# Optimization experiments

Measured on AMD Instinct MI355X. Metric: run time of the kernel, lower is better.

The kernel has to match this reference:

```python
import jax, jax.numpy as jnp
import numpy as np

B, N, NODE_DIM, EMB, T = 16, 256, 5, 128, 4


def _linear_params(key, din, dout):
    kw, kb = jax.random.split(key)
    s = 1.0 / np.sqrt(din)
    w = jax.random.uniform(kw, (din, dout), minval=-s, maxval=s, dtype=jnp.float32)
    b = jax.random.uniform(kb, (dout,), minval=-s, maxval=s, dtype=jnp.float32)
    return w, b


def setup_inputs() -> dict:
    key = jax.random.key(0)
    ks = jax.random.split(key, 10)
    inp = {
        "xv": jax.random.normal(ks[0], (B, N, NODE_DIM), dtype=jnp.float32),
        "Ws": jax.random.uniform(ks[1], (B, N, N), dtype=jnp.float32),
    }
    inp["t1_w"], inp["t1_b"] = _linear_params(ks[2], NODE_DIM, EMB)
    inp["t2_w"], inp["t2_b"] = _linear_params(ks[3], EMB, EMB)
    inp["t3_w"], inp["t3_b"] = _linear_params(ks[4], EMB, EMB)
    inp["t4_w"], inp["t4_b"] = _linear_params(ks[5], 1, EMB)
    inp["t5_w"], inp["t5_b"] = _linear_params(ks[6], 2 * EMB, 1)
    inp["t6_w"], inp["t6_b"] = _linear_params(ks[7], EMB, EMB)
    inp["t7_w"], inp["t7_b"] = _linear_params(ks[8], EMB, EMB)
    inp["layer_w"], inp["layer_b"] = _linear_params(ks[9], EMB, EMB)
    return inp


def reference(xv, Ws, t1_w, t1_b, t2_w, t2_b, t3_w, t3_b, t4_w, t4_b,
              t5_w, t5_b, t6_w, t6_b, t7_w, t7_b, layer_w, layer_b):
    batch, num_nodes = xv.shape[0], xv.shape[1]
    emb = t1_w.shape[1]
    conn = (Ws > 0).astype(xv.dtype)  # [B,N,N]
    # s1 = layer(relu(theta1(xv)))
    s1 = jnp.maximum(xv @ t1_w + t1_b, 0.0) @ layer_w + layer_b  # [B,N,E]
    # s3 = theta3(sum_i relu(theta4(Ws[:,i,j,None])))
    s3_1 = jnp.maximum(Ws[..., None] * t4_w[0] + t4_b, 0.0)  # [B,N,N,E]
    s3 = s3_1.sum(axis=1) @ t3_w + t3_b  # [B,N,E]
    mu = jnp.zeros((batch, num_nodes, emb), dtype=xv.dtype)
    for _ in range(T):
        s2 = jnp.matmul(conn, mu) @ t2_w + t2_b  # [B,N,E]
        mu = jnp.maximum(s1 + s2 + s3, 0.0)
    # global state: theta6 applied to pooled mu, broadcast to all nodes
    global_state = mu.sum(axis=1, keepdims=True) @ t6_w + t6_b  # [B,1,E]
    global_state = jnp.broadcast_to(global_state, mu.shape)  # [B,N,E]
    local_action = mu @ t7_w + t7_b  # [B,N,E]
    out = jnp.maximum(jnp.concatenate([global_state, local_action], axis=2), 0.0)
    return (out @ t5_w + t5_b).squeeze(2)  # [B,N]
```

## Files before the change

### kernel.cpp

```cpp
#include <hip/hip_runtime.h>

#define BATCH 16
#define NN    256
#define E     128
#define NR    (BATCH*NN)
#define ZCAP  8
#define KP    132
#define MAGIC 0x7F3A2B1C

typedef float f4 __attribute__((ext_vector_type(4)));

__global__ __launch_bounds__(1024) void k_all(
    const float* __restrict__ xv,  const float* __restrict__ Ws,
    const float* __restrict__ t1w, const float* __restrict__ t1b,
    const float* __restrict__ t2w, const float* __restrict__ t2b,
    const float* __restrict__ t3w, const float* __restrict__ t3b,
    const float* __restrict__ t4w, const float* __restrict__ t4b,
    const float* __restrict__ t5w, const float* __restrict__ t5b,
    const float* __restrict__ t6w, const float* __restrict__ t6b,
    const float* __restrict__ t7w, const float* __restrict__ t7b,
    const float* __restrict__ lw,  const float* __restrict__ lb,
    float* __restrict__ s13g, float* __restrict__ zmu4g,
    float* __restrict__ s2b3g, float* __restrict__ gsumG,
    int* __restrict__ zcnt, int* __restrict__ doneA, int* __restrict__ flagA,
    float* __restrict__ out)
{
    (void)zmu4g; (void)s2b3g; (void)gsumG; (void)flagA;

    const int blk = blockIdx.x;
    const int b   = blk >> 4;
    const int bt  = blk & 15;
    const int j0  = bt * 16;
    const int r0  = b*NN + j0;
    const int t   = threadIdx.x;
    const int e   = t & 127;
    const int q   = t >> 7;
    const size_t bb = (size_t)b*NN*E;

    __shared__ __align__(16) float s3l[16][KP];
    __shared__ __align__(16) float hsl[16][KP];
    __shared__ __align__(16) float s13l[16][E];
    __shared__ __align__(16) float sQA[8][E];
    __shared__ __align__(16) float sQB[8][E];
    __shared__ __align__(16) float dbuf[E], s2bL[E];
    __shared__ float zmuP[ZCAP][E], zmuN[ZCAP][E];
    __shared__ int   zmap[NN];
    __shared__ int   zlist[ZCAP];
    __shared__ int   nzs;
    __shared__ int   lcnt[16];
    __shared__ float sredO[16][2];
    __shared__ float sg2[2];

    const float* wb = Ws + (size_t)b*NN*NN;
    if (t < 16) lcnt[t] = 0;

    {
        const int jl = t & 15, s = t >> 4;
        const int e4 = (s & 31) * 4, ipart = s >> 5;
        float a0=t4w[e4],a1=t4w[e4+1],a2=t4w[e4+2],a3=t4w[e4+3];
        float c0=t4b[e4],c1=t4b[e4+1],c2=t4b[e4+2],c3=t4b[e4+3];
        float x0=0,x1=0,x2=0,x3=0;
        const float* p = wb + (size_t)(ipart*128)*NN + j0 + jl;
        #pragma unroll 8
        for (int i = 0; i < 128; ++i) {
            float w = p[(size_t)i*NN];
            x0 += fmaxf(w*a0 + c0, 0.f);
            x1 += fmaxf(w*a1 + c1, 0.f);
            x2 += fmaxf(w*a2 + c2, 0.f);
            x3 += fmaxf(w*a3 + c3, 0.f);
        }
        __syncthreads();
        if (ipart == 0) {
            f4 v; v.x=x0; v.y=x1; v.z=x2; v.w=x3;
            *(f4*)&s3l[jl][e4] = v;
        }
        __syncthreads();
        if (ipart == 1) {
            f4 v = *(const f4*)&s3l[jl][e4];
            v.x+=x0; v.y+=x1; v.z+=x2; v.w+=x3;
            *(f4*)&s3l[jl][e4] = v;
        }
    }
    {
        float b1 = t1b[e];
        float w0=t1w[e],w1=t1w[E+e],w2=t1w[2*E+e],w3=t1w[3*E+e],w4=t1w[4*E+e];
        #pragma unroll
        for (int rr = 0; rr < 2; ++rr) {
            const float* x = xv + (size_t)(r0 + q*2 + rr)*5;
            hsl[q*2+rr][e] =
                fmaxf(b1 + x[0]*w0+x[1]*w1+x[2]*w2+x[3]*w3+x[4]*w4, 0.f);
        }
    }
    {
        const int rw = t >> 6, l = t & 63;
        f4 w = *(const f4*)(wb + (size_t)(j0 + rw)*NN + l*4);
        int c = (w.x<=0.f) + (w.y<=0.f) + (w.z<=0.f) + (w.w<=0.f);
        if (c) atomicAdd(&lcnt[rw], c);
    }
    __syncthreads();
    {
        const int jp = q*2;
        float acc0 = 0.f, acc1 = 0.f;
        #pragma unroll 2
        for (int k0 = 0; k0 < E; k0 += 4) {
            f4 h0 = *(const f4*)&hsl[jp][k0];
            f4 h1 = *(const f4*)&hsl[jp+1][k0];
            f4 s0 = *(const f4*)&s3l[jp][k0];
            f4 s1 = *(const f4*)&s3l[jp+1][k0];
            #pragma unroll
            for (int m = 0; m < 4; ++m) {
                float wl = lw[(k0+m)*E + e], w3 = t3w[(k0+m)*E + e];
                acc0 += h0[m]*wl + s0[m]*w3;
                acc1 += h1[m]*wl + s1[m]*w3;
            }
        }
        float bb2 = lb[e] + t3b[e];
        float v0 = acc0 + bb2, v1 = acc1 + bb2;
        s13l[jp][e] = v0;  s13l[jp+1][e] = v1;
        __hip_atomic_store(&s13g[(size_t)(r0+jp)*E + e],   v0,
                           __ATOMIC_RELAXED, __HIP_MEMORY_SCOPE_AGENT);
        __hip_atomic_store(&s13g[(size_t)(r0+jp+1)*E + e], v1,
                           __ATOMIC_RELAXED, __HIP_MEMORY_SCOPE_AGENT);
    }
    if (t < 16)
        __hip_atomic_store(&zcnt[r0 + t], lcnt[t],
                           __ATOMIC_RELAXED, __HIP_MEMORY_SCOPE_AGENT);
    __syncthreads();
    if (t == 0)
        __hip_atomic_store(&doneA[b*16 + bt], MAGIC,
                           __ATOMIC_RELEASE, __HIP_MEMORY_SCOPE_AGENT);

    if (t == 0) {
        int ok = 0, spins = 0;
        while (ok < 16 && spins < (1 << 18)) {
            ok = 0;
            #pragma unroll
            for (int i = 0; i < 16; ++i)
                ok += (__hip_atomic_load(&doneA[b*16+i], __ATOMIC_RELAXED,
                                         __HIP_MEMORY_SCOPE_AGENT) == MAGIC);
            if (ok < 16) __builtin_amdgcn_s_sleep(2);
            ++spins;
        }
        (void)__hip_atomic_load(&doneA[b*16], __ATOMIC_ACQUIRE,
                                __HIP_MEMORY_SCOPE_AGENT);
        nzs = 0;
    }
    if (t < NN) zmap[t] = -1;
    __syncthreads();
    if (t < NN) {
        if (__hip_atomic_load(&zcnt[b*NN + t], __ATOMIC_RELAXED,
                              __HIP_MEMORY_SCOPE_AGENT) > 0) {
            int s = atomicAdd(&nzs, 1);
            if (s < ZCAP) { zlist[s] = t; zmap[t] = s; }
        }
    }
    __syncthreads();
    const int nz = nzs < ZCAP ? nzs : ZCAP;

    float reg[32];
    #pragma unroll
    for (int j = 0; j < 32; ++j)
        reg[j] = __hip_atomic_load(&s13g[bb + (size_t)(q*32+j)*E + e],
                                   __ATOMIC_RELAXED, __HIP_MEMORY_SCOPE_AGENT);

    float s2b_r  = t2b[e];
    float s2bP_r = s2b_r;

    for (int it = 0; it < 4; ++it) {
        if (nz > 0) {
            if (q == 0) s2bL[e] = s2b_r;
            __syncthreads();
            for (int z = 0; z < nz; ++z) {
                int j = zlist[z];
                float cp = 0.f;
                const float* wr = wb + (size_t)j*NN;
                if (it > 0) {
                    #pragma unroll
                    for (int u = 0; u < 32; ++u) {
                        int i = q*32 + u;
                        if (wr[i] <= 0.f) {
                            int zi = zmap[i];
                            cp += (zi >= 0) ? zmuP[zi][e]
                                            : fmaxf(reg[u] + s2bP_r, 0.f);
                        }
                    }
                }
                sQA[q][e] = cp;
                __syncthreads();
                if (q == 0) {
                    float s = 0.f;
                    #pragma unroll
                    for (int qq = 0; qq < 8; ++qq) s += sQA[qq][e];
                    dbuf[e] = s;
                }
                __syncthreads();
                float cb = 0.f;
                #pragma unroll 2
                for (int k = 0; k < E; k += 4) {
                    f4 d = *(const f4*)&dbuf[k];
                    cb += d.x*t2w[(k+0)*E+e] + d.y*t2w[(k+1)*E+e]
                        + d.z*t2w[(k+2)*E+e] + d.w*t2w[(k+3)*E+e];
                }
                if (q == 0) {
                    float sj = __hip_atomic_load(&s13g[bb+(size_t)j*E+e],
                                  __ATOMIC_RELAXED, __HIP_MEMORY_SCOPE_AGENT);
                    zmuN[z][e] = fmaxf(sj + s2b_r - cb, 0.f);
                }
                __syncthreads();
            }
        }

        float csp = 0.f;
        #pragma unroll
        for (int u = 0; u < 32; ++u) csp += fmaxf(reg[u] + s2b_r, 0.f);
        sQA[q][e] = csp;
        __syncthreads();

        const float* W = (it < 3) ? t2w : t6w;
        float pa = 0.f;
        #pragma unroll
        for (int g4 = 0; g4 < 4; ++g4) {
            const int k0 = q*16 + g4*4;
            f4 c = *(const f4*)&sQA[0][k0];
            #pragma unroll
            for (int qq = 1; qq < 8; ++qq) {
                f4 d = *(const f4*)&sQA[qq][k0];
                c.x += d.x; c.y += d.y; c.z += d.z; c.w += d.w;
            }
            if (nz > 0) {
                for (int z = 0; z < nz; ++z) {
                    int j = zlist[z];
                    #pragma unroll
                    for (int m = 0; m < 4; ++m) {
                        float sj = __hip_atomic_load(
                            &s13g[bb+(size_t)j*E + k0 + m],
                            __ATOMIC_RELAXED, __HIP_MEMORY_SCOPE_AGENT);
                        c[m] += zmuN[z][k0+m] - fmaxf(sj + s2bL[k0+m], 0.f);
                    }
                }
            }
            pa += c.x*W[(k0+0)*E+e] + c.y*W[(k0+1)*E+e]
                + c.z*W[(k0+2)*E+e] + c.w*W[(k0+3)*E+e];
        }
        sQB[q][e] = pa;
        s2bP_r = s2b_r;
        if (nz > 0 && q == 0)
            for (int z = 0; z < nz; ++z) zmuP[z][e] = zmuN[z][e];
        __syncthreads();

        if (it < 3) {
            float s = t2b[e];
            #pragma unroll
            for (int qq = 0; qq < 8; ++qq) s += sQB[qq][e];
            s2b_r = s;
        }
    }

    if (q == 0) {
        float g = t6b[e];
        #pragma unroll
        for (int qq = 0; qq < 8; ++qq) g += sQB[qq][e];
        float v = fmaxf(g, 0.f) * t5w[e];
        #pragma unroll
        for (int off = 32; off; off >>= 1) v += __shfl_down(v, off, 64);
        if ((t & 63) == 0) sg2[t >> 6] = v;
    }
    {
        #pragma unroll
        for (int rr = 0; rr < 2; ++rr) {
            int row = q*2 + rr;
            int zi  = zmap[j0 + row];
            float v = (zi >= 0) ? zmuP[zi][e]
                                : fmaxf(s13l[row][e] + s2b_r, 0.f);
            hsl[row][e] = v;
        }
    }
    __syncthreads();

    {
        const int jp = q*2;
        float a0 = 0.f, a1 = 0.f;
        #pragma unroll 2
        for (int k0 = 0; k0 < E; k0 += 4) {
            f4 m0 = *(const f4*)&hsl[jp][k0];
            f4 m1 = *(const f4*)&hsl[jp+1][k0];
            #pragma unroll
            for (int m = 0; m < 4; ++m) {
                float w7 = t7w[(k0+m)*E + e];
                a0 += m0[m]*w7;
                a1 += m1[m]*w7;
            }
        }
        float b7 = t7b[e], w5 = t5w[E+e];
        float v0 = fmaxf(a0 + b7, 0.f) * w5;
        float v1 = fmaxf(a1 + b7, 0.f) * w5;
        #pragma unroll
        for (int off = 32; off; off >>= 1) {
            v0 += __shfl_down(v0, off, 64);
            v1 += __shfl_down(v1, off, 64);
        }
        if ((t & 63) == 0) {
            sredO[jp][e >> 6]   = v0;
            sredO[jp+1][e >> 6] = v1;
        }
    }
    __syncthreads();
    if (t < 16)
        out[r0 + t] = sredO[t][0] + sredO[t][1] + sg2[0] + sg2[1] + t5b[0];
}

extern "C" void kernel_launch(void* const* d_in, const int* in_sizes, int n_in,
                              void* d_out, int out_size, void* d_ws, size_t ws_size,
                              hipStream_t stream) {
    const float* xv  = (const float*)d_in[0];
    const float* Ws  = (const float*)d_in[1];
    const float* t1w = (const float*)d_in[2];  const float* t1b = (const float*)d_in[3];
    const float* t2w = (const float*)d_in[4];  const float* t2b = (const float*)d_in[5];
    const float* t3w = (const float*)d_in[6];  const float* t3b = (const float*)d_in[7];
    const float* t4w = (const float*)d_in[8];  const float* t4b = (const float*)d_in[9];
    const float* t5w = (const float*)d_in[10]; const float* t5b = (const float*)d_in[11];
    const float* t6w = (const float*)d_in[12]; const float* t6b = (const float*)d_in[13];
    const float* t7w = (const float*)d_in[14]; const float* t7b = (const float*)d_in[15];
    const float* lw  = (const float*)d_in[16]; const float* lb  = (const float*)d_in[17];
    float* outp = (float*)d_out;

    float* ws = (float*)d_ws;
    const int RE = NR*E;
    float* s13g  = ws;
    float* zmu4g = ws + RE;
    float* s2b3g = ws + 2*RE;
    float* gsumG = s2b3g + BATCH*E;
    int*   zcnt  = (int*)(gsumG + 64);
    int*   doneA = zcnt + NR + 64;
    int*   flagA = doneA + BATCH*16 + 64;

    k_all<<<256, 1024, 0, stream>>>(xv, Ws, t1w, t1b, t2w, t2b, t3w, t3b,
                                    t4w, t4b, t5w, t5b, t6w, t6b, t7w, t7b,
                                    lw, lb, s13g, zmu4g, s2b3g, gsumG,
                                    zcnt, doneA, flagA, outp);
}
```

Baseline: 132.3 us.

## Split each batch across 32 blocks of 8 rows for twice the grid

Each block now owns 8 node rows instead of 16, and the grid doubles from 256 to 512 blocks. The per-batch spin barrier now waits on 32 blocks instead of 16. The s3 column sum is rewritten so each thread sums all 256 rows for one (row, embedding) pair. The zero-count step now uses a wave shuffle reduction instead of shared atomics. The launch bound asks for 8 waves per EU so two blocks can share a CU. That bound caps registers and may cause spills, and the spin barrier only works if all 512 blocks are resident at once.

```diff
diff --git a/kernel.cpp b/kernel.cpp
--- a/kernel.cpp
+++ b/kernel.cpp
@@ -5,12 +5,14 @@
 #define E     128
 #define NR    (BATCH*NN)
 #define ZCAP  8
+#define TR    8
+#define NT    32
 #define KP    132
 #define MAGIC 0x7F3A2B1C
 
 typedef float f4 __attribute__((ext_vector_type(4)));
 
-__global__ __launch_bounds__(1024) void k_all(
+__global__ __launch_bounds__(1024, 8) void k_all(
     const float* __restrict__ xv,  const float* __restrict__ Ws,
     const float* __restrict__ t1w, const float* __restrict__ t1b,
     const float* __restrict__ t2w, const float* __restrict__ t2b,
@@ -28,18 +30,18 @@
     (void)zmu4g; (void)s2b3g; (void)gsumG; (void)flagA;
 
     const int blk = blockIdx.x;
-    const int b   = blk >> 4;
-    const int bt  = blk & 15;
-    const int j0  = bt * 16;
+    const int b   = blk >> 5;
+    const int bt  = blk & 31;
+    const int j0  = bt * TR;
     const int r0  = b*NN + j0;
     const int t   = threadIdx.x;
     const int e   = t & 127;
     const int q   = t >> 7;
     const size_t bb = (size_t)b*NN*E;
 
-    __shared__ __align__(16) float s3l[16][KP];
-    __shared__ __align__(16) float hsl[16][KP];
-    __shared__ __align__(16) float s13l[16][E];
+    __shared__ __align__(16) float s3l[TR][KP];
+    __shared__ __align__(16) float hsl[TR][KP];
+    __shared__ __align__(16) float s13l[TR][E];
     __shared__ __align__(16) float sQA[8][E];
     __shared__ __align__(16) float sQB[8][E];
     __shared__ __align__(16) float dbuf[E], s2bL[E];
@@ -47,101 +49,74 @@
     __shared__ int   zmap[NN];
     __shared__ int   zlist[ZCAP];
     __shared__ int   nzs;
-    __shared__ int   lcnt[16];
-    __shared__ float sredO[16][2];
+    __shared__ int   lcnt[TR];
+    __shared__ float sredO[TR][2];
     __shared__ float sg2[2];
 
     const float* wb = Ws + (size_t)b*NN*NN;
-    if (t < 16) lcnt[t] = 0;
-
-    {
-        const int jl = t & 15, s = t >> 4;
-        const int e4 = (s & 31) * 4, ipart = s >> 5;
-        float a0=t4w[e4],a1=t4w[e4+1],a2=t4w[e4+2],a3=t4w[e4+3];
-        float c0=t4b[e4],c1=t4b[e4+1],c2=t4b[e4+2],c3=t4b[e4+3];
-        float x0=0,x1=0,x2=0,x3=0;
-        const float* p = wb + (size_t)(ipart*128)*NN + j0 + jl;
-        #pragma unroll 8
-        for (int i = 0; i < 128; ++i) {
-            float w = p[(size_t)i*NN];
-            x0 += fmaxf(w*a0 + c0, 0.f);
-            x1 += fmaxf(w*a1 + c1, 0.f);
-            x2 += fmaxf(w*a2 + c2, 0.f);
-            x3 += fmaxf(w*a3 + c3, 0.f);
-        }
-        __syncthreads();
-        if (ipart == 0) {
-            f4 v; v.x=x0; v.y=x1; v.z=x2; v.w=x3;
-            *(f4*)&s3l[jl][e4] = v;
-        }
-        __syncthreads();
-        if (ipart == 1) {
-            f4 v = *(const f4*)&s3l[jl][e4];
-            v.x+=x0; v.y+=x1; v.z+=x2; v.w+=x3;
-            *(f4*)&s3l[jl][e4] = v;
-        }
-    }
+
     {
         float b1 = t1b[e];
         float w0=t1w[e],w1=t1w[E+e],w2=t1w[2*E+e],w3=t1w[3*E+e],w4=t1w[4*E+e];
-        #pragma unroll
-        for (int rr = 0; rr < 2; ++rr) {
-            const float* x = xv + (size_t)(r0 + q*2 + rr)*5;
-            hsl[q*2+rr][e] =
-                fmaxf(b1 + x[0]*w0+x[1]*w1+x[2]*w2+x[3]*w3+x[4]*w4, 0.f);
-        }
-    }
-    {
-        const int rw = t >> 6, l = t & 63;
-        f4 w = *(const f4*)(wb + (size_t)(j0 + rw)*NN + l*4);
-        int c = (w.x<=0.f) + (w.y<=0.f) + (w.z<=0.f) + (w.w<=0.f);
-        if (c) atomicAdd(&lcnt[rw], c);
-    }
-    __syncthreads();
-    {
-        const int jp = q*2;
-        float acc0 = 0.f, acc1 = 0.f;
+        const float* x = xv + (size_t)(r0 + q)*5;
+        hsl[q][e] = fmaxf(b1 + x[0]*w0+x[1]*w1+x[2]*w2+x[3]*w3+x[4]*w4, 0.f);
+    }
+    {
+        const int jl = t & 7, se = t >> 3;
+        float a = t4w[se], c = t4b[se];
+        float x = 0.f;
+        const float* p = wb + j0 + jl;
+        #pragma unroll 8
+        for (int i = 0; i < NN; ++i)
+            x += fmaxf(p[(size_t)i*NN]*a + c, 0.f);
+        s3l[jl][se] = x;
+    }
+    {
+        const int w = t >> 6, l = t & 63;
+        if (w < TR) {
+            f4 v = *(const f4*)(wb + (size_t)(j0 + w)*NN + l*4);
+            int c = (v.x<=0.f) + (v.y<=0.f) + (v.z<=0.f) + (v.w<=0.f);
+            #pragma unroll
+            for (int off = 32; off; off >>= 1) c += __shfl_down(c, off, 64);
+            if (l == 0) lcnt[w] = c;
+        }
+    }
+    __syncthreads();
+    {
+        float acc = 0.f;
         #pragma unroll 2
         for (int k0 = 0; k0 < E; k0 += 4) {
-            f4 h0 = *(const f4*)&hsl[jp][k0];
-            f4 h1 = *(const f4*)&hsl[jp+1][k0];
-            f4 s0 = *(const f4*)&s3l[jp][k0];
-            f4 s1 = *(const f4*)&s3l[jp+1][k0];
-            #pragma unroll
-            for (int m = 0; m < 4; ++m) {
-                float wl = lw[(k0+m)*E + e], w3 = t3w[(k0+m)*E + e];
-                acc0 += h0[m]*wl + s0[m]*w3;
-                acc1 += h1[m]*wl + s1[m]*w3;
-            }
-        }
-        float bb2 = lb[e] + t3b[e];
-        float v0 = acc0 + bb2, v1 = acc1 + bb2;
-        s13l[jp][e] = v0;  s13l[jp+1][e] = v1;
-        __hip_atomic_store(&s13g[(size_t)(r0+jp)*E + e],   v0,
+            f4 h = *(const f4*)&hsl[q][k0];
+            f4 s = *(const f4*)&s3l[q][k0];
+            #pragma unroll
+            for (int m = 0; m < 4; ++m)
+                acc += h[m]*lw[(k0+m)*E + e] + s[m]*t3w[(k0+m)*E + e];
+        }
+        float v = acc + lb[e] + t3b[e];
+        s13l[q][e] = v;
+        __hip_atomic_store(&s13g[(size_t)(r0+q)*E + e], v,
                            __ATOMIC_RELAXED, __HIP_MEMORY_SCOPE_AGENT);
-        __hip_atomic_store(&s13g[(size_t)(r0+jp+1)*E + e], v1,
-                           __ATOMIC_RELAXED, __HIP_MEMORY_SCOPE_AGENT);
-    }
-    if (t < 16)
+    }
+    if (t < TR)
         __hip_atomic_store(&zcnt[r0 + t], lcnt[t],
                            __ATOMIC_RELAXED, __HIP_MEMORY_SCOPE_AGENT);
     __syncthreads();
     if (t == 0)
-        __hip_atomic_store(&doneA[b*16 + bt], MAGIC,
+        __hip_atomic_store(&doneA[b*NT + bt], MAGIC,
                            __ATOMIC_RELEASE, __HIP_MEMORY_SCOPE_AGENT);
 
     if (t == 0) {
         int ok = 0, spins = 0;
-        while (ok < 16 && spins < (1 << 18)) {
+        while (ok < NT && spins < (1 << 18)) {
             ok = 0;
             #pragma unroll
-            for (int i = 0; i < 16; ++i)
-                ok += (__hip_atomic_load(&doneA[b*16+i], __ATOMIC_RELAXED,
+            for (int i = 0; i < NT; ++i)
+                ok += (__hip_atomic_load(&doneA[b*NT+i], __ATOMIC_RELAXED,
                                          __HIP_MEMORY_SCOPE_AGENT) == MAGIC);
-            if (ok < 16) __builtin_amdgcn_s_sleep(2);
+            if (ok < NT) __builtin_amdgcn_s_sleep(2);
             ++spins;
         }
-        (void)__hip_atomic_load(&doneA[b*16], __ATOMIC_ACQUIRE,
+        (void)__hip_atomic_load(&doneA[b*NT], __ATOMIC_ACQUIRE,
                                 __HIP_MEMORY_SCOPE_AGENT);
         nzs = 0;
     }
@@ -266,46 +241,29 @@
         if ((t & 63) == 0) sg2[t >> 6] = v;
     }
     {
-        #pragma unroll
-        for (int rr = 0; rr < 2; ++rr) {
-            int row = q*2 + rr;
-            int zi  = zmap[j0 + row];
-            float v = (zi >= 0) ? zmuP[zi][e]
-                                : fmaxf(s13l[row][e] + s2b_r, 0.f);
-            hsl[row][e] = v;
-        }
-    }
-    __syncthreads();
-
-    {
-        const int jp = q*2;
-        float a0 = 0.f, a1 = 0.f;
+        int zi  = zmap[j0 + q];
+        float v = (zi >= 0) ? zmuP[zi][e]
+                            : fmaxf(s13l[q][e] + s2b_r, 0.f);
+        hsl[q][e] = v;
+    }
+    __syncthreads();
+
+    {
+        float a0 = 0.f;
         #pragma unroll 2
         for (int k0 = 0; k0 < E; k0 += 4) {
-            f4 m0 = *(const f4*)&hsl[jp][k0];
-            f4 m1 = *(const f4*)&hsl[jp+1][k0];
-            #pragma unroll
-            for (int m = 0; m < 4; ++m) {
-                float w7 = t7w[(k0+m)*E + e];
-                a0 += m0[m]*w7;
-                a1 += m1[m]*w7;
-            }
-        }
-        float b7 = t7b[e], w5 = t5w[E+e];
-        float v0 = fmaxf(a0 + b7, 0.f) * w5;
-        float v1 = fmaxf(a1 + b7, 0.f) * w5;
-        #pragma unroll
-        for (int off = 32; off; off >>= 1) {
-            v0 += __shfl_down(v0, off, 64);
-            v1 += __shfl_down(v1, off, 64);
-        }
-        if ((t & 63) == 0) {
-            sredO[jp][e >> 6]   = v0;
-            sredO[jp+1][e >> 6] = v1;
-        }
-    }
-    __syncthreads();
-    if (t < 16)
+            f4 m0 = *(const f4*)&hsl[q][k0];
+            #pragma unroll
+            for (int m = 0; m < 4; ++m)
+                a0 += m0[m]*t7w[(k0+m)*E + e];
+        }
+        float v0 = fmaxf(a0 + t7b[e], 0.f) * t5w[E+e];
+        #pragma unroll
+        for (int off = 32; off; off >>= 1) v0 += __shfl_down(v0, off, 64);
+        if ((t & 63) == 0) sredO[q][(t >> 6) & 1] = v0;
+    }
+    __syncthreads();
+    if (t < TR)
         out[r0 + t] = sredO[t][0] + sredO[t][1] + sg2[0] + sg2[1] + t5b[0];
 }
 
@@ -332,9 +290,9 @@
     float* gsumG = s2b3g + BATCH*E;
     int*   zcnt  = (int*)(gsumG + 64);
     int*   doneA = zcnt + NR + 64;
-    int*   flagA = doneA + BATCH*16 + 64;
-
-    k_all<<<256, 1024, 0, stream>>>(xv, Ws, t1w, t1b, t2w, t2b, t3w, t3b,
+    int*   flagA = doneA + BATCH*NT + 64;
+
+    k_all<<<512, 1024, 0, stream>>>(xv, Ws, t1w, t1b, t2w, t2b, t3w, t3b,
                                     t4w, t4b, t5w, t5b, t6w, t6b, t7w, t7b,
                                     lw, lb, s13g, zmu4g, s2b3g, gsumG,
                                     zcnt, doneA, flagA, outp);
```

After: 245.4 us. 1.85x slower.

## Stage Ws column tile in LDS for s3 reduction and use wave-reduced zero counts

Applied to the files above, without the earlier changes.

The Ws column slab for the block's 16 nodes is now copied once into shared memory with coalesced vector loads. The relu-sum for s3 then reads it from LDS, each thread covering two nodes and one embedding lane over all 256 rows. Before, every thread made strided global loads over half the rows and the two halves were merged with an extra sync step. Per-row zero counts now use a wavefront shuffle reduction instead of shared atomics. The cost is 16 KB more shared memory, which may affect occupancy, plus a longer serial inner loop per thread.

```diff
diff --git a/kernel.cpp b/kernel.cpp
--- a/kernel.cpp
+++ b/kernel.cpp
@@ -9,6 +9,7 @@
 #define MAGIC 0x7F3A2B1C
 
 typedef float f4 __attribute__((ext_vector_type(4)));
+typedef float f2 __attribute__((ext_vector_type(2)));
 
 __global__ __launch_bounds__(1024) void k_all(
     const float* __restrict__ xv,  const float* __restrict__ Ws,
@@ -37,6 +38,7 @@
     const int q   = t >> 7;
     const size_t bb = (size_t)b*NN*E;
 
+    __shared__ __align__(16) float wst[NN][16];
     __shared__ __align__(16) float s3l[16][KP];
     __shared__ __align__(16) float hsl[16][KP];
     __shared__ __align__(16) float s13l[16][E];
@@ -52,34 +54,10 @@
     __shared__ float sg2[2];
 
     const float* wb = Ws + (size_t)b*NN*NN;
-    if (t < 16) lcnt[t] = 0;
-
-    {
-        const int jl = t & 15, s = t >> 4;
-        const int e4 = (s & 31) * 4, ipart = s >> 5;
-        float a0=t4w[e4],a1=t4w[e4+1],a2=t4w[e4+2],a3=t4w[e4+3];
-        float c0=t4b[e4],c1=t4b[e4+1],c2=t4b[e4+2],c3=t4b[e4+3];
-        float x0=0,x1=0,x2=0,x3=0;
-        const float* p = wb + (size_t)(ipart*128)*NN + j0 + jl;
-        #pragma unroll 8
-        for (int i = 0; i < 128; ++i) {
-            float w = p[(size_t)i*NN];
-            x0 += fmaxf(w*a0 + c0, 0.f);
-            x1 += fmaxf(w*a1 + c1, 0.f);
-            x2 += fmaxf(w*a2 + c2, 0.f);
-            x3 += fmaxf(w*a3 + c3, 0.f);
-        }
-        __syncthreads();
-        if (ipart == 0) {
-            f4 v; v.x=x0; v.y=x1; v.z=x2; v.w=x3;
-            *(f4*)&s3l[jl][e4] = v;
-        }
-        __syncthreads();
-        if (ipart == 1) {
-            f4 v = *(const f4*)&s3l[jl][e4];
-            v.x+=x0; v.y+=x1; v.z+=x2; v.w+=x3;
-            *(f4*)&s3l[jl][e4] = v;
-        }
+
+    {
+        const int i = t >> 2, jq = (t & 3) * 4;
+        *(f4*)&wst[i][jq] = *(const f4*)(wb + (size_t)i*NN + j0 + jq);
     }
     {
         float b1 = t1b[e];
@@ -92,10 +70,27 @@
         }
     }
     {
-        const int rw = t >> 6, l = t & 63;
-        f4 w = *(const f4*)(wb + (size_t)(j0 + rw)*NN + l*4);
-        int c = (w.x<=0.f) + (w.y<=0.f) + (w.z<=0.f) + (w.w<=0.f);
-        if (c) atomicAdd(&lcnt[rw], c);
+        const int w = t >> 6, l = t & 63;
+        f4 v = *(const f4*)(wb + (size_t)(j0 + w)*NN + l*4);
+        int c = (v.x<=0.f) + (v.y<=0.f) + (v.z<=0.f) + (v.w<=0.f);
+        #pragma unroll
+        for (int off = 32; off; off >>= 1) c += __shfl_down(c, off, 64);
+        if (l == 0) lcnt[w] = c;
+    }
+    __syncthreads();
+    {
+        const int jp = 2*q;
+        const float a = t4w[e], c = t4b[e];
+        float x0 = 0.f, x1 = 0.f;
+        const f2* wp = (const f2*)&wst[0][jp];
+        #pragma unroll 8
+        for (int i = 0; i < NN; ++i) {
+            f2 w = wp[i*8];
+            x0 += fmaxf(w.x*a + c, 0.f);
+            x1 += fmaxf(w.y*a + c, 0.f);
+        }
+        s3l[jp][e]   = x0;
+        s3l[jp+1][e] = x1;
     }
     __syncthreads();
     {
```

Measured after the change: 134.4 us. Within noise of the previous version (+1.6%).
